# Performance work log

Hardware: AMD Instinct MI355X
Metric: run time of the kernel (lower is better)

The kernel has to match this reference:

```python
import jax, jax.numpy as jnp
import numpy as np

N_TOKENS = 16384
D_IN = 1024
D_OUT = 1024
N_EXPS = 8


def setup_inputs() -> dict:
    key = jax.random.key(0)
    k1, k2, k3, k4 = jax.random.split(key, 4)
    embs = jax.random.normal(k1, (N_TOKENS, D_IN), dtype=jnp.float32)
    exps_T = jax.random.normal(k2, (D_IN, N_EXPS), dtype=jnp.float32) * 0.02
    expert_bias = jax.random.normal(k3, (N_EXPS, D_IN), dtype=jnp.float32) * 0.02
    expert_W = jax.random.normal(k4, (N_EXPS, D_OUT, D_IN), dtype=jnp.float32) * 0.02
    return {"embs": embs, "exps_T": exps_T, "expert_bias": expert_bias, "expert_W": expert_W}


def reference(embs, exps_T, expert_bias, expert_W):
    # Gating (eval path: no noise, no rel_gate)
    scores = embs @ exps_T                      # [n, e]
    exps_sco = jax.nn.softmax(scores, axis=-1)  # [n, e]
    # All-experts dense evaluation: (embs - bias_e) @ W_e^T for each expert e
    shifted = embs[:, None, :] - expert_bias[None, :, :]        # [n, e, d]
    expert_outputs = jnp.einsum('ned,eod->neo', shifted, expert_W)  # [n, e, o]
    # Softmax-weighted reduction over experts
    multi_out = jnp.einsum('ne,neo->no', exps_sco, expert_outputs)  # [n, o]
    return (multi_out, expert_outputs)
```

## Files before the change

kernel.cpp:

```cpp
#include <hip/hip_runtime.h>
#include <hip/hip_bf16.h>
#include <stdint.h>

#define N_TOKENS 16384
#define D_IN 1024
#define D_OUT 1024
#define N_EXPS 8

typedef __bf16 bf16x8 __attribute__((ext_vector_type(8)));
typedef float f32x4 __attribute__((ext_vector_type(4)));

typedef __attribute__((address_space(1))) void gvoid_t;
typedef __attribute__((address_space(3))) void lvoid_t;

__device__ __forceinline__ void async_copy16(void* lds, const void* g) {
    __builtin_amdgcn_global_load_lds((gvoid_t*)g, (lvoid_t*)lds, 16, 0, 0);
}

__device__ __forceinline__ unsigned short f2bf_u16(float f) {
    union { __hip_bfloat16 h; unsigned short u; } cv;
    cv.h = __float2bfloat16(f);
    return cv.u;
}

__global__ __launch_bounds__(256) void gate_convert_kernel(
    const float* __restrict__ embs, const float* __restrict__ expsT,
    unsigned short* __restrict__ embs_bf, float* __restrict__ probs) {
    const int row  = blockIdx.x * 4 + (threadIdx.x >> 6);
    const int lane = threadIdx.x & 63;
    const float* er = embs + (size_t)row * D_IN;

    float s[N_EXPS];
#pragma unroll
    for (int e = 0; e < N_EXPS; ++e) s[e] = 0.f;

#pragma unroll
    for (int j = 0; j < 4; ++j) {
        const int chunk = j * 64 + lane;
        const float4 v = ((const float4*)er)[chunk];
        const int d = chunk * 4;
        const float vv[4] = {v.x, v.y, v.z, v.w};
#pragma unroll
        for (int q = 0; q < 4; ++q) {
            const float4 t0 = ((const float4*)(expsT + (size_t)(d + q) * N_EXPS))[0];
            const float4 t1 = ((const float4*)(expsT + (size_t)(d + q) * N_EXPS))[1];
            s[0] += vv[q] * t0.x; s[1] += vv[q] * t0.y;
            s[2] += vv[q] * t0.z; s[3] += vv[q] * t0.w;
            s[4] += vv[q] * t1.x; s[5] += vv[q] * t1.y;
            s[6] += vv[q] * t1.z; s[7] += vv[q] * t1.w;
        }
        ushort4 u;
        u.x = f2bf_u16(v.x); u.y = f2bf_u16(v.y);
        u.z = f2bf_u16(v.z); u.w = f2bf_u16(v.w);
        ((ushort4*)embs_bf)[(size_t)row * 256 + chunk] = u;
    }

#pragma unroll
    for (int off = 32; off; off >>= 1) {
#pragma unroll
        for (int e = 0; e < N_EXPS; ++e) s[e] += __shfl_xor(s[e], off, 64);
    }

    float mx = s[0];
#pragma unroll
    for (int e = 1; e < N_EXPS; ++e) mx = fmaxf(mx, s[e]);
    float pe[N_EXPS];
    float sum = 0.f;
#pragma unroll
    for (int e = 0; e < N_EXPS; ++e) { pe[e] = __expf(s[e] - mx); sum += pe[e]; }
    const float inv = 1.f / sum;
    if (lane == 0) {
#pragma unroll
        for (int e = 0; e < N_EXPS; ++e) probs[(size_t)row * N_EXPS + e] = pe[e] * inv;
    }
}

__global__ __launch_bounds__(256) void wconv_kernel(
    const float* __restrict__ W, const float* __restrict__ bias,
    unsigned short* __restrict__ Wbf, float* __restrict__ cvec) {
    const int gw   = blockIdx.x * 4 + (threadIdx.x >> 6);
    const int lane = threadIdx.x & 63;
    const int e    = gw >> 10;
    const float* wr = W + (size_t)gw * D_IN;
    const float* br = bias + (size_t)e * D_IN;

    float dot = 0.f;
#pragma unroll
    for (int j = 0; j < 4; ++j) {
        const int chunk = j * 64 + lane;
        const float4 w4 = ((const float4*)wr)[chunk];
        const float4 b4 = ((const float4*)br)[chunk];
        dot += w4.x * b4.x + w4.y * b4.y + w4.z * b4.z + w4.w * b4.w;
        ushort4 u;
        u.x = f2bf_u16(w4.x); u.y = f2bf_u16(w4.y);
        u.z = f2bf_u16(w4.z); u.w = f2bf_u16(w4.w);
        ((ushort4*)Wbf)[(size_t)gw * 256 + chunk] = u;
    }
#pragma unroll
    for (int off = 32; off; off >>= 1) dot += __shfl_xor(dot, off, 64);
    if (lane == 0) cvec[gw] = dot;
}

__global__ __launch_bounds__(512, 2) void moe_gemm_kernel(
    const __hip_bfloat16* __restrict__ Abf, const __hip_bfloat16* __restrict__ Wbf,
    const float* __restrict__ probs, const float* __restrict__ cvec,
    float* __restrict__ out_multi, float* __restrict__ out_exp) {
    constexpr int BM = 256, BN = 128, BK = 64;
    constexpr int NIT    = N_EXPS * (D_IN / BK);
    constexpr int ABYTES = BM * BK * 2;
    constexpr int BBYTES = BN * BK * 2;
    constexpr int BUFB   = ABYTES + BBYTES;
    extern __shared__ char smem[];
    float* p_lds = (float*)(smem + 3 * BUFB);
    float* c_lds = (float*)(smem + 3 * BUFB + 8192);

    const int tid  = threadIdx.x;
    const int lane = tid & 63;
    const int lm   = lane & 15;
    const int lq   = lane >> 4;
    const int wave = tid >> 6;
    const int wr   = wave >> 1;
    const int wc   = wave & 1;
    const int nT   = blockIdx.x & 7;
    const int mT   = blockIdx.x >> 3;
    const int m0   = mT * BM;
    const int n0   = nT * BN;

    const int trow = tid >> 3;
    const int tcol = (tid & 7) ^ (trow & 7);
    const __hip_bfloat16* gA = Abf + (size_t)(m0 + trow) * D_IN + tcol * 8;
    const __hip_bfloat16* gB = Wbf + (size_t)(n0 + trow) * D_IN + tcol * 8;
    const int ldsoff = (tid & ~63) << 4;

    auto stage_h = [&](int it, int buf, int half) {
        const int e  = it >> 4;
        const int ko = (it & 15) * BK;
        char* base = smem + buf * BUFB;
        const __hip_bfloat16* gAk = gA + ko;
        const __hip_bfloat16* gBk = gB + (size_t)e * ((size_t)D_OUT * D_IN) + ko;
        if (half == 0) {
            async_copy16(base + 0 * 8192 + ldsoff, gAk + 0 * 64 * D_IN);
            async_copy16(base + 1 * 8192 + ldsoff, gAk + 1 * 64 * D_IN);
            async_copy16(base + ABYTES + 0 * 8192 + ldsoff, gBk);
        } else {
            async_copy16(base + 2 * 8192 + ldsoff, gAk + 2 * 64 * D_IN);
            async_copy16(base + 3 * 8192 + ldsoff, gAk + 3 * 64 * D_IN);
            async_copy16(base + ABYTES + 1 * 8192 + ldsoff, gBk + 64 * D_IN);
        }
    };

    for (int i = tid; i < N_EXPS * BM; i += 512)
        p_lds[(i >> 8) * 256 + (i & 255)] = probs[(size_t)(m0 + (i & 255)) * N_EXPS + (i >> 8)];
    for (int i = tid; i < N_EXPS * BN; i += 512)
        c_lds[(i >> 7) * 128 + (i & 127)] = cvec[(size_t)(i >> 7) * D_OUT + n0 + (i & 127)];

    stage_h(0, 0, 0); stage_h(0, 0, 1);
    stage_h(1, 1, 0); stage_h(1, 1, 1);

    const int axor = (lm & 7) << 4;
    int a_off0[4], a_off1[4], b_off0[4], b_off1[4];
#pragma unroll
    for (int t = 0; t < 4; ++t) {
        const int ra = (wr * 64 + t * 16 + lm) * 128 + lq * 16;
        const int rb = (wc * 64 + t * 16 + lm) * 128 + lq * 16;
        a_off0[t] = (ra +  0) ^ axor;
        a_off1[t] = (ra + 64) ^ axor;
        b_off0[t] = ABYTES + ((rb +  0) ^ axor);
        b_off1[t] = ABYTES + ((rb + 64) ^ axor);
    }

    f32x4 acc[4][4];
    f32x4 multi[4][4];
    const f32x4 fzero = {0.f, 0.f, 0.f, 0.f};
#pragma unroll
    for (int ti = 0; ti < 4; ++ti)
#pragma unroll
        for (int tj = 0; tj < 4; ++tj) { acc[ti][tj] = fzero; multi[ti][tj] = fzero; }

    auto epilogue = [&](int e) {
        float cv[4];
#pragma unroll
        for (int tj = 0; tj < 4; ++tj) cv[tj] = c_lds[e * 128 + wc * 64 + tj * 16 + lm];
#pragma unroll
        for (int ti = 0; ti < 4; ++ti) {
#pragma unroll
            for (int r = 0; r < 4; ++r) {
                const int rloc = wr * 64 + ti * 16 + lq * 4 + r;
                const int grow = m0 + rloc;
                const float p = p_lds[e * 256 + rloc];
                float* orow = out_exp + ((size_t)grow * N_EXPS + e) * D_OUT + n0 + wc * 64;
#pragma unroll
                for (int tj = 0; tj < 4; ++tj) {
                    const float val = acc[ti][tj][r] - cv[tj];
                    __builtin_nontemporal_store(val, &orow[tj * 16 + lm]);
                    multi[ti][tj][r] = fmaf(p, val, multi[ti][tj][r]);
                }
            }
        }
    };

    asm volatile("s_waitcnt lgkmcnt(0)" ::: "memory");
    asm volatile("s_waitcnt vmcnt(6)" ::: "memory");
    __builtin_amdgcn_s_barrier();
    __builtin_amdgcn_sched_barrier(0);

    int cur = 0;
    for (int it = 0; it < NIT; ++it) {
        const char* buf = smem + cur * BUFB;
        const int nb2 = (cur == 0) ? 2 : cur - 1;

        {
            bf16x8 a[4], b[4];
#pragma unroll
            for (int t = 0; t < 4; ++t) a[t] = *(const bf16x8*)(buf + a_off0[t]);
#pragma unroll
            for (int t = 0; t < 4; ++t) b[t] = *(const bf16x8*)(buf + b_off0[t]);
            if (it + 2 < NIT) stage_h(it + 2, nb2, 0);
            __builtin_amdgcn_sched_barrier(0);
            __builtin_amdgcn_s_barrier();
            __builtin_amdgcn_sched_barrier(0);
            __builtin_amdgcn_s_setprio(1);
#pragma unroll
            for (int ti = 0; ti < 4; ++ti)
#pragma unroll
                for (int tj = 0; tj < 4; ++tj)
                    acc[ti][tj] = __builtin_amdgcn_mfma_f32_16x16x32_bf16(
                        a[ti], b[tj], acc[ti][tj], 0, 0, 0);
            __builtin_amdgcn_s_setprio(0);
            __builtin_amdgcn_sched_barrier(0);
            __builtin_amdgcn_s_barrier();
        }

        {
            bf16x8 a[4], b[4];
#pragma unroll
            for (int t = 0; t < 4; ++t) a[t] = *(const bf16x8*)(buf + a_off1[t]);
#pragma unroll
            for (int t = 0; t < 4; ++t) b[t] = *(const bf16x8*)(buf + b_off1[t]);
            if (it + 2 < NIT) stage_h(it + 2, nb2, 1);
            __builtin_amdgcn_sched_barrier(0);
            __builtin_amdgcn_s_barrier();
            __builtin_amdgcn_sched_barrier(0);
            __builtin_amdgcn_s_setprio(1);
#pragma unroll
            for (int ti = 0; ti < 4; ++ti)
#pragma unroll
                for (int tj = 0; tj < 4; ++tj)
                    acc[ti][tj] = __builtin_amdgcn_mfma_f32_16x16x32_bf16(
                        a[ti], b[tj], acc[ti][tj], 0, 0, 0);
            __builtin_amdgcn_s_setprio(0);
            __builtin_amdgcn_sched_barrier(0);
        }

        if (it + 2 < NIT) {
            asm volatile("s_waitcnt vmcnt(6)" ::: "memory");
        } else if (it + 1 < NIT) {
            asm volatile("s_waitcnt vmcnt(0)" ::: "memory");
        }
        __builtin_amdgcn_s_barrier();

        if ((it & 15) == 15) {
            epilogue(it >> 4);
#pragma unroll
            for (int ti = 0; ti < 4; ++ti)
#pragma unroll
                for (int tj = 0; tj < 4; ++tj) acc[ti][tj] = fzero;
        }
        cur = (cur == 2) ? 0 : cur + 1;
    }

#pragma unroll
    for (int ti = 0; ti < 4; ++ti) {
#pragma unroll
        for (int r = 0; r < 4; ++r) {
            const int grow = m0 + wr * 64 + ti * 16 + lq * 4 + r;
            float* mrow = out_multi + (size_t)grow * D_OUT + n0 + wc * 64;
#pragma unroll
            for (int tj = 0; tj < 4; ++tj)
                __builtin_nontemporal_store(multi[ti][tj][r], &mrow[tj * 16 + lm]);
        }
    }
}

extern "C" void kernel_launch(void* const* d_in, const int* in_sizes, int n_in,
                              void* d_out, int out_size, void* d_ws, size_t ws_size,
                              hipStream_t stream) {
    const float* embs  = (const float*)d_in[0];
    const float* expsT = (const float*)d_in[1];
    const float* bias  = (const float*)d_in[2];
    const float* W     = (const float*)d_in[3];

    float* out_multi = (float*)d_out;
    float* out_exp   = (float*)d_out + (size_t)N_TOKENS * D_OUT;

    char* ws = (char*)d_ws;
    unsigned short* embs_bf = (unsigned short*)ws;
    unsigned short* W_bf    = (unsigned short*)(ws + 33554432);
    float*          probs   = (float*)(ws + 33554432 + 16777216);
    float*          cvec    = (float*)(ws + 33554432 + 16777216 + 524288);

    constexpr int SMEM_BYTES = 3 * (256 * 64 * 2 + 128 * 64 * 2) + 8192 + 4096;
    static bool configured = false;
    if (!configured) {
        hipFuncSetAttribute(reinterpret_cast<const void*>(moe_gemm_kernel),
                            hipFuncAttributeMaxDynamicSharedMemorySize, SMEM_BYTES);
        configured = true;
    }

    gate_convert_kernel<<<N_TOKENS / 4, 256, 0, stream>>>(embs, expsT, embs_bf, probs);
    wconv_kernel<<<(N_EXPS * D_OUT) / 4, 256, 0, stream>>>(W, bias, W_bf, cvec);
    moe_gemm_kernel<<<(N_TOKENS / 256) * (D_OUT / 128), 512, SMEM_BYTES, stream>>>(
        (const __hip_bfloat16*)embs_bf, (const __hip_bfloat16*)W_bf,
        probs, cvec, out_multi, out_exp);
}
```

Measured before the change: 1.021 ms.

## Process four experts per pass sharing each A tile across expert weights

Restructures the GEMM main loop so each K-step loads one A tile (128x32) and the B tiles of four experts, running MFMAs for all four from the same A fragments. The block tile shrinks from 256x128 to 128x128 with BK=32, the wave layout becomes 2x4, and the grid doubles. A is now read from global memory twice per block instead of eight times, cutting A traffic and LDS reads per MFMA. In exchange each wave holds four expert accumulators, which raises register pressure, and the output is written in bursts of four experts at a time.

```diff
diff --git a/kernel.cpp b/kernel.cpp
--- a/kernel.cpp
+++ b/kernel.cpp
@@ -105,179 +105,162 @@
     const __hip_bfloat16* __restrict__ Abf, const __hip_bfloat16* __restrict__ Wbf,
     const float* __restrict__ probs, const float* __restrict__ cvec,
     float* __restrict__ out_multi, float* __restrict__ out_exp) {
-    constexpr int BM = 256, BN = 128, BK = 64;
-    constexpr int NIT    = N_EXPS * (D_IN / BK);
+    constexpr int BM = 128, BN = 128, BK = 32, EG = 4;
+    constexpr int NIT    = (N_EXPS / EG) * (D_IN / BK);
     constexpr int ABYTES = BM * BK * 2;
-    constexpr int BBYTES = BN * BK * 2;
-    constexpr int BUFB   = ABYTES + BBYTES;
+    constexpr int EBYTES = BN * BK * 2;
+    constexpr int BUFB   = ABYTES + EG * EBYTES;
     extern __shared__ char smem[];
     float* p_lds = (float*)(smem + 3 * BUFB);
-    float* c_lds = (float*)(smem + 3 * BUFB + 8192);
+    float* c_lds = (float*)(smem + 3 * BUFB + 4096);
 
     const int tid  = threadIdx.x;
     const int lane = tid & 63;
     const int lm   = lane & 15;
     const int lq   = lane >> 4;
     const int wave = tid >> 6;
-    const int wr   = wave >> 1;
-    const int wc   = wave & 1;
+    const int wr   = wave >> 2;
+    const int wc   = wave & 3;
     const int nT   = blockIdx.x & 7;
     const int mT   = blockIdx.x >> 3;
     const int m0   = mT * BM;
     const int n0   = nT * BN;
 
-    const int trow = tid >> 3;
-    const int tcol = (tid & 7) ^ (trow & 7);
+    const int trow = tid >> 2;
+    const int tcol = (tid & 3) ^ ((tid >> 3) & 3);
     const __hip_bfloat16* gA = Abf + (size_t)(m0 + trow) * D_IN + tcol * 8;
     const __hip_bfloat16* gB = Wbf + (size_t)(n0 + trow) * D_IN + tcol * 8;
-    const int ldsoff = (tid & ~63) << 4;
-
-    auto stage_h = [&](int it, int buf, int half) {
-        const int e  = it >> 4;
-        const int ko = (it & 15) * BK;
+    const int ldsoff = (tid & ~63) * 16;
+
+    auto stage = [&](int it, int buf) {
+        const int pass = it >> 5;
+        const int ko   = (it & 31) * BK;
         char* base = smem + buf * BUFB;
-        const __hip_bfloat16* gAk = gA + ko;
-        const __hip_bfloat16* gBk = gB + (size_t)e * ((size_t)D_OUT * D_IN) + ko;
-        if (half == 0) {
-            async_copy16(base + 0 * 8192 + ldsoff, gAk + 0 * 64 * D_IN);
-            async_copy16(base + 1 * 8192 + ldsoff, gAk + 1 * 64 * D_IN);
-            async_copy16(base + ABYTES + 0 * 8192 + ldsoff, gBk);
-        } else {
-            async_copy16(base + 2 * 8192 + ldsoff, gAk + 2 * 64 * D_IN);
-            async_copy16(base + 3 * 8192 + ldsoff, gAk + 3 * 64 * D_IN);
-            async_copy16(base + ABYTES + 1 * 8192 + ldsoff, gBk + 64 * D_IN);
-        }
+        async_copy16(base + ldsoff, gA + ko);
+        const __hip_bfloat16* gBk = gB + ko + (size_t)(pass * EG) * ((size_t)D_OUT * D_IN);
+#pragma unroll
+        for (int el = 0; el < EG; ++el)
+            async_copy16(base + ABYTES + el * EBYTES + ldsoff,
+                         gBk + (size_t)el * ((size_t)D_OUT * D_IN));
     };
 
     for (int i = tid; i < N_EXPS * BM; i += 512)
-        p_lds[(i >> 8) * 256 + (i & 255)] = probs[(size_t)(m0 + (i & 255)) * N_EXPS + (i >> 8)];
+        p_lds[(i >> 7) * 128 + (i & 127)] = probs[(size_t)(m0 + (i & 127)) * N_EXPS + (i >> 7)];
     for (int i = tid; i < N_EXPS * BN; i += 512)
         c_lds[(i >> 7) * 128 + (i & 127)] = cvec[(size_t)(i >> 7) * D_OUT + n0 + (i & 127)];
-
-    stage_h(0, 0, 0); stage_h(0, 0, 1);
-    stage_h(1, 1, 0); stage_h(1, 1, 1);
-
-    const int axor = (lm & 7) << 4;
-    int a_off0[4], a_off1[4], b_off0[4], b_off1[4];
-#pragma unroll
-    for (int t = 0; t < 4; ++t) {
-        const int ra = (wr * 64 + t * 16 + lm) * 128 + lq * 16;
-        const int rb = (wc * 64 + t * 16 + lm) * 128 + lq * 16;
-        a_off0[t] = (ra +  0) ^ axor;
-        a_off1[t] = (ra + 64) ^ axor;
-        b_off0[t] = ABYTES + ((rb +  0) ^ axor);
-        b_off1[t] = ABYTES + ((rb + 64) ^ axor);
-    }
-
-    f32x4 acc[4][4];
-    f32x4 multi[4][4];
+    __builtin_amdgcn_sched_barrier(0);
+
+    stage(0, 0);
+    stage(1, 1);
+
+    const int sw     = (lq ^ ((lm >> 1) & 3)) * 16;
+    const int a_base = (wr * 64 + lm) * 64 + sw;
+    const int b_base = ABYTES + (wc * 32 + lm) * 64 + sw;
+
+    f32x4 acc[EG][4][2];
+    f32x4 multi[4][2];
     const f32x4 fzero = {0.f, 0.f, 0.f, 0.f};
 #pragma unroll
-    for (int ti = 0; ti < 4; ++ti)
-#pragma unroll
-        for (int tj = 0; tj < 4; ++tj) { acc[ti][tj] = fzero; multi[ti][tj] = fzero; }
-
-    auto epilogue = [&](int e) {
-        float cv[4];
-#pragma unroll
-        for (int tj = 0; tj < 4; ++tj) cv[tj] = c_lds[e * 128 + wc * 64 + tj * 16 + lm];
-#pragma unroll
-        for (int ti = 0; ti < 4; ++ti) {
-#pragma unroll
-            for (int r = 0; r < 4; ++r) {
-                const int rloc = wr * 64 + ti * 16 + lq * 4 + r;
-                const int grow = m0 + rloc;
-                const float p = p_lds[e * 256 + rloc];
-                float* orow = out_exp + ((size_t)grow * N_EXPS + e) * D_OUT + n0 + wc * 64;
-#pragma unroll
-                for (int tj = 0; tj < 4; ++tj) {
-                    const float val = acc[ti][tj][r] - cv[tj];
-                    __builtin_nontemporal_store(val, &orow[tj * 16 + lm]);
-                    multi[ti][tj][r] = fmaf(p, val, multi[ti][tj][r]);
+    for (int el = 0; el < EG; ++el)
+#pragma unroll
+        for (int mi = 0; mi < 4; ++mi)
+#pragma unroll
+            for (int nj = 0; nj < 2; ++nj) acc[el][mi][nj] = fzero;
+#pragma unroll
+    for (int mi = 0; mi < 4; ++mi)
+#pragma unroll
+        for (int nj = 0; nj < 2; ++nj) multi[mi][nj] = fzero;
+
+    auto epilogue = [&](int ebase) {
+#pragma unroll
+        for (int el = 0; el < EG; ++el) {
+            const int e = ebase + el;
+            float cv[2];
+#pragma unroll
+            for (int nj = 0; nj < 2; ++nj) cv[nj] = c_lds[e * 128 + wc * 32 + nj * 16 + lm];
+#pragma unroll
+            for (int mi = 0; mi < 4; ++mi) {
+#pragma unroll
+                for (int r = 0; r < 4; ++r) {
+                    const int rloc = wr * 64 + mi * 16 + lq * 4 + r;
+                    const int grow = m0 + rloc;
+                    const float p = p_lds[e * 128 + rloc];
+                    float* orow = out_exp + ((size_t)grow * N_EXPS + e) * D_OUT + n0 + wc * 32;
+#pragma unroll
+                    for (int nj = 0; nj < 2; ++nj) {
+                        const float val = acc[el][mi][nj][r] - cv[nj];
+                        __builtin_nontemporal_store(val, &orow[nj * 16 + lm]);
+                        multi[mi][nj][r] = fmaf(p, val, multi[mi][nj][r]);
+                    }
                 }
             }
         }
     };
 
     asm volatile("s_waitcnt lgkmcnt(0)" ::: "memory");
-    asm volatile("s_waitcnt vmcnt(6)" ::: "memory");
+    asm volatile("s_waitcnt vmcnt(5)" ::: "memory");
     __builtin_amdgcn_s_barrier();
     __builtin_amdgcn_sched_barrier(0);
 
     int cur = 0;
     for (int it = 0; it < NIT; ++it) {
         const char* buf = smem + cur * BUFB;
-        const int nb2 = (cur == 0) ? 2 : cur - 1;
-
-        {
-            bf16x8 a[4], b[4];
-#pragma unroll
-            for (int t = 0; t < 4; ++t) a[t] = *(const bf16x8*)(buf + a_off0[t]);
-#pragma unroll
-            for (int t = 0; t < 4; ++t) b[t] = *(const bf16x8*)(buf + b_off0[t]);
-            if (it + 2 < NIT) stage_h(it + 2, nb2, 0);
-            __builtin_amdgcn_sched_barrier(0);
-            __builtin_amdgcn_s_barrier();
-            __builtin_amdgcn_sched_barrier(0);
-            __builtin_amdgcn_s_setprio(1);
-#pragma unroll
-            for (int ti = 0; ti < 4; ++ti)
-#pragma unroll
-                for (int tj = 0; tj < 4; ++tj)
-                    acc[ti][tj] = __builtin_amdgcn_mfma_f32_16x16x32_bf16(
-                        a[ti], b[tj], acc[ti][tj], 0, 0, 0);
-            __builtin_amdgcn_s_setprio(0);
-            __builtin_amdgcn_sched_barrier(0);
-            __builtin_amdgcn_s_barrier();
-        }
-
-        {
-            bf16x8 a[4], b[4];
-#pragma unroll
-            for (int t = 0; t < 4; ++t) a[t] = *(const bf16x8*)(buf + a_off1[t]);
-#pragma unroll
-            for (int t = 0; t < 4; ++t) b[t] = *(const bf16x8*)(buf + b_off1[t]);
-            if (it + 2 < NIT) stage_h(it + 2, nb2, 1);
-            __builtin_amdgcn_sched_barrier(0);
-            __builtin_amdgcn_s_barrier();
-            __builtin_amdgcn_sched_barrier(0);
-            __builtin_amdgcn_s_setprio(1);
-#pragma unroll
-            for (int ti = 0; ti < 4; ++ti)
-#pragma unroll
-                for (int tj = 0; tj < 4; ++tj)
-                    acc[ti][tj] = __builtin_amdgcn_mfma_f32_16x16x32_bf16(
-                        a[ti], b[tj], acc[ti][tj], 0, 0, 0);
-            __builtin_amdgcn_s_setprio(0);
-            __builtin_amdgcn_sched_barrier(0);
-        }
+        const int nb2 = (cur >= 1) ? cur - 1 : 2;
+
+        bf16x8 a[4], b[EG][2];
+#pragma unroll
+        for (int mi = 0; mi < 4; ++mi)
+            a[mi] = *(const bf16x8*)(buf + a_base + mi * 1024);
+#pragma unroll
+        for (int el = 0; el < EG; ++el)
+#pragma unroll
+            for (int nj = 0; nj < 2; ++nj)
+                b[el][nj] = *(const bf16x8*)(buf + b_base + el * EBYTES + nj * 1024);
+        if (it + 2 < NIT) stage(it + 2, nb2);
+
+        __builtin_amdgcn_sched_barrier(0);
+        __builtin_amdgcn_s_barrier();
+        __builtin_amdgcn_sched_barrier(0);
+        __builtin_amdgcn_s_setprio(1);
+#pragma unroll
+        for (int el = 0; el < EG; ++el)
+#pragma unroll
+            for (int mi = 0; mi < 4; ++mi)
+#pragma unroll
+                for (int nj = 0; nj < 2; ++nj)
+                    acc[el][mi][nj] = __builtin_amdgcn_mfma_f32_16x16x32_bf16(
+                        a[mi], b[el][nj], acc[el][mi][nj], 0, 0, 0);
+        __builtin_amdgcn_s_setprio(0);
+        __builtin_amdgcn_sched_barrier(0);
 
         if (it + 2 < NIT) {
-            asm volatile("s_waitcnt vmcnt(6)" ::: "memory");
+            asm volatile("s_waitcnt vmcnt(5)" ::: "memory");
         } else if (it + 1 < NIT) {
             asm volatile("s_waitcnt vmcnt(0)" ::: "memory");
         }
         __builtin_amdgcn_s_barrier();
 
-        if ((it & 15) == 15) {
-            epilogue(it >> 4);
-#pragma unroll
-            for (int ti = 0; ti < 4; ++ti)
-#pragma unroll
-                for (int tj = 0; tj < 4; ++tj) acc[ti][tj] = fzero;
+        if ((it & 31) == 31) {
+            epilogue((it >> 5) * EG);
+#pragma unroll
+            for (int el = 0; el < EG; ++el)
+#pragma unroll
+                for (int mi = 0; mi < 4; ++mi)
+#pragma unroll
+                    for (int nj = 0; nj < 2; ++nj) acc[el][mi][nj] = fzero;
         }
         cur = (cur == 2) ? 0 : cur + 1;
     }
 
 #pragma unroll
-    for (int ti = 0; ti < 4; ++ti) {
+    for (int mi = 0; mi < 4; ++mi) {
 #pragma unroll
         for (int r = 0; r < 4; ++r) {
-            const int grow = m0 + wr * 64 + ti * 16 + lq * 4 + r;
-            float* mrow = out_multi + (size_t)grow * D_OUT + n0 + wc * 64;
-#pragma unroll
-            for (int tj = 0; tj < 4; ++tj)
-                __builtin_nontemporal_store(multi[ti][tj][r], &mrow[tj * 16 + lm]);
+            const int grow = m0 + wr * 64 + mi * 16 + lq * 4 + r;
+            float* mrow = out_multi + (size_t)grow * D_OUT + n0 + wc * 32;
+#pragma unroll
+            for (int nj = 0; nj < 2; ++nj)
+                __builtin_nontemporal_store(multi[mi][nj][r], &mrow[nj * 16 + lm]);
         }
     }
 }
@@ -299,7 +282,7 @@
     float*          probs   = (float*)(ws + 33554432 + 16777216);
     float*          cvec    = (float*)(ws + 33554432 + 16777216 + 524288);
 
-    constexpr int SMEM_BYTES = 3 * (256 * 64 * 2 + 128 * 64 * 2) + 8192 + 4096;
+    constexpr int SMEM_BYTES = 3 * 40960 + 4096 + 4096;
     static bool configured = false;
     if (!configured) {
         hipFuncSetAttribute(reinterpret_cast<const void*>(moe_gemm_kernel),
@@ -309,7 +292,7 @@
 
     gate_convert_kernel<<<N_TOKENS / 4, 256, 0, stream>>>(embs, expsT, embs_bf, probs);
     wconv_kernel<<<(N_EXPS * D_OUT) / 4, 256, 0, stream>>>(W, bias, W_bf, cvec);
-    moe_gemm_kernel<<<(N_TOKENS / 256) * (D_OUT / 128), 512, SMEM_BYTES, stream>>>(
+    moe_gemm_kernel<<<(N_TOKENS / 128) * (D_OUT / 128), 512, SMEM_BYTES, stream>>>(
         (const __hip_bfloat16*)embs_bf, (const __hip_bfloat16*)W_bf,
         probs, cvec, out_multi, out_exp);
 }
```

New measurement: 971.7 us. 1.05x faster.
